# Performance work log

Measured on AMD Instinct MI355X. Metric: run time of the kernel, lower is better.

Reference implementation:

```python
import jax, jax.numpy as jnp
import numpy as np

DMODEL = 1024
NHEAD = 16
DHEAD = DMODEL // NHEAD

def _layernorm(x, g, b, eps=1e-5):
    mu = jnp.mean(x, axis=-1, keepdims=True)
    var = jnp.var(x, axis=-1, keepdims=True)
    return (x - mu) * jax.lax.rsqrt(var + eps) * g + b

def setup_inputs() -> dict:
    key = jax.random.key(0)
    ks = jax.random.split(key, 12)
    b, lq, lv, d = 2, 2048, 2048, DMODEL
    s = 1.0 / np.sqrt(d)
    return {
        "q": jax.random.normal(ks[0], (b, lq, d), jnp.float32),
        "k": jax.random.normal(ks[1], (b, lv, d), jnp.float32),
        "v": jax.random.normal(ks[2], (b, lv, d), jnp.float32),
        "qln_g": jnp.ones((d,), jnp.float32),
        "qln_b": jnp.zeros((d,), jnp.float32),
        "kvln_g": jnp.ones((d,), jnp.float32),
        "kvln_b": jnp.zeros((d,), jnp.float32),
        "Wq": jax.random.normal(ks[3], (d, d), jnp.float32) * s,
        "Wk": jax.random.normal(ks[4], (d, d), jnp.float32) * s,
        "Wv": jax.random.normal(ks[5], (d, d), jnp.float32) * s,
        "Wg": jax.random.normal(ks[6], (d, d), jnp.float32) * s,
        "bg": jnp.zeros((d,), jnp.float32),
        "Wo": jax.random.normal(ks[7], (d, d), jnp.float32) * s,
    }

def reference(q, k, v, qln_g, qln_b, kvln_g, kvln_b, Wq, Wk, Wv, Wg, bg, Wo):
    b, lq, d = q.shape
    lv = v.shape[1]
    qn = _layernorm(q, qln_g, qln_b)           # [b, lq, d]
    q_ = qn @ Wq.T
    kk = _layernorm(k, kvln_g, kvln_b) @ Wk.T
    vv = _layernorm(v, kvln_g, kvln_b) @ Wv.T
    qh = q_.reshape(b, lq, NHEAD, DHEAD)       # bqhd
    kh = kk.reshape(b, lv, NHEAD, DHEAD)
    vh = vv.reshape(b, lv, NHEAD, DHEAD)
    scores = jnp.einsum('bqhd,bkhd->bhqk', qh, kh) / np.sqrt(DHEAD)
    attn = jax.nn.softmax(scores, axis=-1)
    y = jnp.einsum('bhqk,bkhd->bqhd', attn, vh).reshape(b, lq, d)
    g = jax.nn.sigmoid(qn @ Wg.T + bg)
    return (y * g) @ Wo.T
```

## Files before the change

### kernel.cpp

```cpp
#include <hip/hip_runtime.h>
#include <hip/hip_bf16.h>

#define DMODEL 1024
#define NHEAD  16
#define DHEAD  64
#define BATCH  2
#define LQ     2048
#define LV     2048
#define ROWS   (BATCH*LQ)
#define WELEMS (DMODEL*DMODEL)
#define BH     (BATCH*NHEAD)

typedef short bf16x8 __attribute__((ext_vector_type(8)));
typedef float f32x4  __attribute__((ext_vector_type(4)));

__device__ __forceinline__ float bf2f(unsigned short s) {
    union { unsigned u; float f; } v; v.u = ((unsigned)s) << 16;
    return v.f;
}
__device__ __forceinline__ unsigned pk_bf(float a, float b) {
    union { __hip_bfloat162 h; unsigned u; } c;
    c.h = __float22bfloat162_rn(make_float2(a, b));
    return c.u;
}

__device__ __forceinline__ void cp16_g2l(const void* g, void* l) {
    __builtin_amdgcn_global_load_lds(
        (const __attribute__((address_space(1))) void*)g,
        (__attribute__((address_space(3))) void*)l,
        16, 0, 0);
}

#define QSCALE (0.125f * 1.4426950408889634f)

__global__ __launch_bounds__(256) void prep_kernel(
    const float* q, const float* k, const float* v,
    const float* qg, const float* qb, const float* kvg, const float* kvb,
    const float* Wq, const float* Wk, const float* Wv, const float* Wg, const float* Wo,
    unsigned short* qn, unsigned short* kn, unsigned short* vn, unsigned short* wb)
{
    __shared__ float rs[4], rq[4];
    int z = blockIdx.y;
    if (z < 5) {
        if (blockIdx.x >= WELEMS / 1024) return;
        const float* srcs[5] = {Wq, Wk, Wv, Wg, Wo};
        const float* s = srcs[z];
        unsigned short* d = wb + (size_t)z * WELEMS;
        int i = (blockIdx.x * 256 + threadIdx.x) * 4;
        float4 x = *(const float4*)(s + i);
        uint2 o = make_uint2(pk_bf(x.x, x.y), pk_bf(x.z, x.w));
        *(uint2*)(d + i) = o;
        return;
    }
    int row = blockIdx.x;
    const float *x, *gp, *bp; unsigned short* o;
    if      (z == 5) { x = q; gp = qg;  bp = qb;  o = qn; }
    else if (z == 6) { x = k; gp = kvg; bp = kvb; o = kn; }
    else             { x = v; gp = kvg; bp = kvb; o = vn; }

    int col = threadIdx.x * 4;
    float4 xv = *(const float4*)(x + (size_t)row * DMODEL + col);
    float s  = xv.x + xv.y + xv.z + xv.w;
    float sq = xv.x*xv.x + xv.y*xv.y + xv.z*xv.z + xv.w*xv.w;
    #pragma unroll
    for (int off = 1; off < 64; off <<= 1) { s += __shfl_xor(s, off); sq += __shfl_xor(sq, off); }

    int wave = threadIdx.x >> 6, lane = threadIdx.x & 63;
    if (lane == 0) { rs[wave] = s; rq[wave] = sq; }
    __syncthreads();
    float ts = rs[0] + rs[1] + rs[2] + rs[3];
    float tq = rq[0] + rq[1] + rq[2] + rq[3];
    float mu  = ts * (1.0f / DMODEL);
    float var = tq * (1.0f / DMODEL) - mu * mu;
    float inv = rsqrtf(var + 1e-5f);

    float4 gv = *(const float4*)(gp + col);
    float4 bv = *(const float4*)(bp + col);
    float r0 = (xv.x - mu) * inv * gv.x + bv.x;
    float r1 = (xv.y - mu) * inv * gv.y + bv.y;
    float r2 = (xv.z - mu) * inv * gv.z + bv.z;
    float r3 = (xv.w - mu) * inv * gv.w + bv.w;
    *(uint2*)(o + (size_t)row * DMODEL + col) = make_uint2(pk_bf(r0, r1), pk_bf(r2, r3));
}

template<int MODE>
__device__ __forceinline__ void gemm_bt_core(
    const unsigned short* A, const unsigned short* Bw,
    unsigned short* Obf, float* Of32, const float* bias, float scale,
    unsigned short* Al, unsigned short* Bl, int bm, int bn)
{
    int tid  = threadIdx.x;
    int wave = tid >> 6, lane = tid & 63, quad = lane >> 4, L = lane & 15;
    int wm = wave >> 1, wn = wave & 1;

    int srow = wave * 16 + (lane >> 2);
    int scol = (lane & 3) * 8;
    const unsigned short* gA = A  + (size_t)(bm * 128 + srow) * DMODEL + scol;
    const unsigned short* gB = Bw + (size_t)(bn * 128 + srow) * DMODEL + scol;
    int lofs0 = wave * 16 * 32;
    int lofs1 = (64 + wave * 16) * 32;

    f32x4 acc[4][4];
    #pragma unroll
    for (int i = 0; i < 4; ++i)
        #pragma unroll
        for (int j = 0; j < 4; ++j) acc[i][j] = (f32x4){0.f, 0.f, 0.f, 0.f};

    cp16_g2l(gA,               Al + lofs0);
    cp16_g2l(gA + 64 * DMODEL, Al + lofs1);
    cp16_g2l(gB,               Bl + lofs0);
    cp16_g2l(gB + 64 * DMODEL, Bl + lofs1);

    int buf = 0;
    for (int k0 = 0; k0 < DMODEL; k0 += 32, buf ^= 1) {
        __syncthreads();
        if (k0 + 32 < DMODEL) {
            int nb = (buf ^ 1) * (128 * 32);
            cp16_g2l(gA + k0 + 32,               Al + nb + lofs0);
            cp16_g2l(gA + 64 * DMODEL + k0 + 32, Al + nb + lofs1);
            cp16_g2l(gB + k0 + 32,               Bl + nb + lofs0);
            cp16_g2l(gB + 64 * DMODEL + k0 + 32, Bl + nb + lofs1);
        }
        const unsigned short* Ab = Al + buf * (128 * 32);
        const unsigned short* Bb = Bl + buf * (128 * 32);
        bf16x8 af[4], bfr[4];
        #pragma unroll
        for (int i = 0; i < 4; ++i)
            af[i] = *(const bf16x8*)&Ab[(wm * 64 + i * 16 + L) * 32 + quad * 8];
        #pragma unroll
        for (int j = 0; j < 4; ++j)
            bfr[j] = *(const bf16x8*)&Bb[(wn * 64 + j * 16 + L) * 32 + quad * 8];
        #pragma unroll
        for (int i = 0; i < 4; ++i)
            #pragma unroll
            for (int j = 0; j < 4; ++j) {
                if (MODE == 3)
                    acc[i][j] = __builtin_amdgcn_mfma_f32_16x16x32_bf16(af[i], bfr[j], acc[i][j], 0, 0, 0);
                else
                    acc[i][j] = __builtin_amdgcn_mfma_f32_16x16x32_bf16(bfr[j], af[i], acc[i][j], 0, 0, 0);
            }
    }

    #pragma unroll
    for (int i = 0; i < 4; ++i) {
        #pragma unroll
        for (int j = 0; j < 4; ++j) {
            f32x4 a = acc[i][j];
            if (MODE == 3) {
                int gcol  = bn * 128 + wn * 64 + j * 16 + L;
                int grow0 = bm * 128 + wm * 64 + i * 16 + quad * 4;
                int b = grow0 >> 11, key0 = grow0 & 2047;
                int h = gcol >> 6,   dd   = gcol & 63;
                uint2 o = make_uint2(pk_bf(a[0], a[1]), pk_bf(a[2], a[3]));
                *(uint2*)&Obf[(((size_t)(b * NHEAD + h) * DHEAD + dd) << 11) + key0] = o;
            } else {
                int grow  = bm * 128 + wm * 64 + i * 16 + L;
                int gcol0 = bn * 128 + wn * 64 + j * 16 + quad * 4;
                size_t idx = (size_t)grow * DMODEL + gcol0;
                if (MODE == 0) {
                    uint2 o = make_uint2(pk_bf(a[0] * scale, a[1] * scale),
                                         pk_bf(a[2] * scale, a[3] * scale));
                    *(uint2*)&Obf[idx] = o;
                } else if (MODE == 1) {
                    float4 bv = *(const float4*)&bias[gcol0];
                    float s0 = 1.0f / (1.0f + __expf(-(a[0] + bv.x)));
                    float s1 = 1.0f / (1.0f + __expf(-(a[1] + bv.y)));
                    float s2 = 1.0f / (1.0f + __expf(-(a[2] + bv.z)));
                    float s3 = 1.0f / (1.0f + __expf(-(a[3] + bv.w)));
                    *(uint2*)&Obf[idx] = make_uint2(pk_bf(s0, s1), pk_bf(s2, s3));
                } else {
                    *(f32x4*)&Of32[idx] = a;
                }
            }
        }
    }
}

__device__ __forceinline__ void xcd_map(int& bm, int& bn) {
    int f = blockIdx.y * 8 + blockIdx.x;
    int xcd = f & 7, s = f >> 3;
    bn = s & 7;
    bm = ((s >> 3) << 3) | xcd;
}

__global__ __launch_bounds__(256) void gemm_batched_kernel(
    const unsigned short* qn, const unsigned short* kn, const unsigned short* vn,
    const unsigned short* wb,
    unsigned short* qs, unsigned short* kkp, unsigned short* vt, unsigned short* gate,
    const float* bg)
{
    __shared__ __align__(16) unsigned short Al[2 * 128 * 32];
    __shared__ __align__(16) unsigned short Bl[2 * 128 * 32];
    int bm, bn; xcd_map(bm, bn);
    switch (blockIdx.z) {
        case 0:  gemm_bt_core<0>(qn, wb + 0 * WELEMS, qs,   nullptr, nullptr, QSCALE, Al, Bl, bm, bn); break;
        case 1:  gemm_bt_core<0>(kn, wb + 1 * WELEMS, kkp,  nullptr, nullptr, 1.0f,   Al, Bl, bm, bn); break;
        case 2:  gemm_bt_core<3>(vn, wb + 2 * WELEMS, vt,   nullptr, nullptr, 1.0f,   Al, Bl, bm, bn); break;
        default: gemm_bt_core<1>(qn, wb + 3 * WELEMS, gate, nullptr, bg,      1.0f,   Al, Bl, bm, bn); break;
    }
}

__global__ __launch_bounds__(256) void gemm_f32out_kernel(
    const unsigned short* A, const unsigned short* Bw, float* O)
{
    __shared__ __align__(16) unsigned short Al[2 * 128 * 32];
    __shared__ __align__(16) unsigned short Bl[2 * 128 * 32];
    int bm, bn; xcd_map(bm, bn);
    gemm_bt_core<2>(A, Bw, nullptr, O, nullptr, 1.0f, Al, Bl, bm, bn);
}

__global__ __launch_bounds__(256, 4) void attn_kernel(
    const unsigned short* qs, const unsigned short* kk, const unsigned short* vt,
    const unsigned short* gate, unsigned short* yg)
{
    __shared__ __align__(16) unsigned short Kl[2 * 64 * 64];
    __shared__ __align__(16) unsigned short Vl[2 * 64 * 64];

    int tid  = threadIdx.x;
    int wave = tid >> 6, lane = tid & 63, quad = lane >> 4, L = lane & 15;

    int f  = blockIdx.y * 32 + blockIdx.x;
    int bh = (f & 7) * 4 + ((f >> 3) & 3);
    int qt = f >> 5;
    int bb = bh >> 4, h = bh & 15;
    int q0 = qt * 64;

    const unsigned short* Qb =
        qs + ((size_t)(bb * LQ + q0 + wave * 16 + L)) * DMODEL + h * DHEAD;
    bf16x8 aq0 = *(const bf16x8*)(Qb + quad * 8);
    bf16x8 aq1 = *(const bf16x8*)(Qb + 32 + quad * 8);

    f32x4 acc[4];
    #pragma unroll
    for (int nt = 0; nt < 4; ++nt) acc[nt] = (f32x4){0.f, 0.f, 0.f, 0.f};
    f32x4 lacc = (f32x4){0.f, 0.f, 0.f, 0.f};
    bf16x8 ones;
    #pragma unroll
    for (int j = 0; j < 8; ++j) ones[j] = (short)0x3F80;

    int rloc = lane >> 3;
    int c16  = (lane & 7) ^ rloc;
    int key0 = (wave & 1) * 32 + (rloc >> 2) * 8 + (wave >> 1) * 4 + (rloc & 3);

    const unsigned short* gK = kk + (size_t)bb * LV * DMODEL + h * DHEAD
                                  + (size_t)key0 * DMODEL + c16 * 8;
    const unsigned short* gV = vt + ((size_t)((bb * NHEAD + h) * DHEAD
                                  + wave * 16 + rloc)) * LV + c16 * 8;
    char* KlB = (char*)Kl;
    char* VlB = (char*)Vl;
    int dst0 = wave * 2048;

    cp16_g2l(gK,               KlB + dst0);
    cp16_g2l(gK + 16 * DMODEL, KlB + dst0 + 1024);
    cp16_g2l(gV,               VlB + dst0);
    cp16_g2l(gV + 8 * LV,      VlB + dst0 + 1024);

    int sl0 = (quad ^ (L & 7)) * 8;
    int buf = 0;
    for (int it = 0; it < LV / 64; ++it, buf ^= 1) {
        __syncthreads();
        if (it + 1 < LV / 64) {
            gK += 64 * DMODEL; gV += 64;
            int nb = (buf ^ 1) * 8192 + dst0;
            cp16_g2l(gK,               KlB + nb);
            cp16_g2l(gK + 16 * DMODEL, KlB + nb + 1024);
            cp16_g2l(gV,               VlB + nb);
            cp16_g2l(gV + 8 * LV,      VlB + nb + 1024);
        }
        const unsigned short* Kb = Kl + buf * 4096;
        const unsigned short* Vb = Vl + buf * 4096;

        f32x4 zz[4];
        __builtin_amdgcn_s_setprio(1);
        #pragma unroll
        for (int kt = 0; kt < 4; ++kt) {
            bf16x8 bk0 = *(const bf16x8*)&Kb[(kt * 16 + L) * 64 + sl0];
            bf16x8 bk1 = *(const bf16x8*)&Kb[(kt * 16 + L) * 64 + (sl0 ^ 32)];
            f32x4 z = (f32x4){0.f, 0.f, 0.f, 0.f};
            z = __builtin_amdgcn_mfma_f32_16x16x32_bf16(bk0, aq0, z, 0, 0, 0);
            z = __builtin_amdgcn_mfma_f32_16x16x32_bf16(bk1, aq1, z, 0, 0, 0);
            zz[kt] = z;
        }
        __builtin_amdgcn_s_setprio(0);

        union { unsigned u[4]; bf16x8 h; } pa0, pa1;
        pa0.u[0] = pk_bf(__builtin_amdgcn_exp2f(zz[0][0]), __builtin_amdgcn_exp2f(zz[0][1]));
        pa0.u[1] = pk_bf(__builtin_amdgcn_exp2f(zz[0][2]), __builtin_amdgcn_exp2f(zz[0][3]));
        pa0.u[2] = pk_bf(__builtin_amdgcn_exp2f(zz[2][0]), __builtin_amdgcn_exp2f(zz[2][1]));
        pa0.u[3] = pk_bf(__builtin_amdgcn_exp2f(zz[2][2]), __builtin_amdgcn_exp2f(zz[2][3]));
        pa1.u[0] = pk_bf(__builtin_amdgcn_exp2f(zz[1][0]), __builtin_amdgcn_exp2f(zz[1][1]));
        pa1.u[1] = pk_bf(__builtin_amdgcn_exp2f(zz[1][2]), __builtin_amdgcn_exp2f(zz[1][3]));
        pa1.u[2] = pk_bf(__builtin_amdgcn_exp2f(zz[3][0]), __builtin_amdgcn_exp2f(zz[3][1]));
        pa1.u[3] = pk_bf(__builtin_amdgcn_exp2f(zz[3][2]), __builtin_amdgcn_exp2f(zz[3][3]));

        __builtin_amdgcn_s_setprio(1);
        lacc = __builtin_amdgcn_mfma_f32_16x16x32_bf16(ones, pa0.h, lacc, 0, 0, 0);
        lacc = __builtin_amdgcn_mfma_f32_16x16x32_bf16(ones, pa1.h, lacc, 0, 0, 0);
        #pragma unroll
        for (int nt = 0; nt < 4; ++nt) {
            bf16x8 vb0 = *(const bf16x8*)&Vb[(nt * 16 + L) * 64 + sl0];
            bf16x8 vb1 = *(const bf16x8*)&Vb[(nt * 16 + L) * 64 + (sl0 ^ 32)];
            acc[nt] = __builtin_amdgcn_mfma_f32_16x16x32_bf16(vb0, pa0.h, acc[nt], 0, 0, 0);
            acc[nt] = __builtin_amdgcn_mfma_f32_16x16x32_bf16(vb1, pa1.h, acc[nt], 0, 0, 0);
        }
        __builtin_amdgcn_s_setprio(0);
    }

    float inv_l = 1.0f / lacc[0];
    size_t rb = ((size_t)(bb * LQ + q0 + wave * 16 + L)) * DMODEL + h * DHEAD;
    #pragma unroll
    for (int nt = 0; nt < 4; ++nt) {
        size_t idx = rb + nt * 16 + quad * 4;
        ushort4 g = *(const ushort4*)&gate[idx];
        float y0 = acc[nt][0] * inv_l * bf2f(g.x);
        float y1 = acc[nt][1] * inv_l * bf2f(g.y);
        float y2 = acc[nt][2] * inv_l * bf2f(g.z);
        float y3 = acc[nt][3] * inv_l * bf2f(g.w);
        *(uint2*)&yg[idx] = make_uint2(pk_bf(y0, y1), pk_bf(y2, y3));
    }
}

extern "C" void kernel_launch(void* const* d_in, const int* in_sizes, int n_in,
                              void* d_out, int out_size, void* d_ws, size_t ws_size,
                              hipStream_t stream)
{
    const float* q      = (const float*)d_in[0];
    const float* k      = (const float*)d_in[1];
    const float* v      = (const float*)d_in[2];
    const float* qln_g  = (const float*)d_in[3];
    const float* qln_b  = (const float*)d_in[4];
    const float* kvln_g = (const float*)d_in[5];
    const float* kvln_b = (const float*)d_in[6];
    const float* Wq     = (const float*)d_in[7];
    const float* Wk     = (const float*)d_in[8];
    const float* Wv     = (const float*)d_in[9];
    const float* Wg     = (const float*)d_in[10];
    const float* bg     = (const float*)d_in[11];
    const float* Wo     = (const float*)d_in[12];
    float* out = (float*)d_out;

    const size_t T8 = (size_t)ROWS * DMODEL * 2;
    char* ws = (char*)d_ws;
    unsigned short* qn   = (unsigned short*)(ws + 0 * T8);
    unsigned short* kn   = (unsigned short*)(ws + 1 * T8);
    unsigned short* vn   = (unsigned short*)(ws + 2 * T8);
    unsigned short* qs   = (unsigned short*)(ws + 3 * T8);
    unsigned short* kkp  = (unsigned short*)(ws + 4 * T8);
    unsigned short* vt   = (unsigned short*)(ws + 5 * T8);
    unsigned short* gate = (unsigned short*)(ws + 6 * T8);
    unsigned short* yg   = (unsigned short*)(ws + 7 * T8);
    unsigned short* wb   = (unsigned short*)(ws + 8 * T8);

    prep_kernel<<<dim3(ROWS, 8), 256, 0, stream>>>(
        q, k, v, qln_g, qln_b, kvln_g, kvln_b, Wq, Wk, Wv, Wg, Wo, qn, kn, vn, wb);
    gemm_batched_kernel<<<dim3(DMODEL / 128, ROWS / 128, 4), 256, 0, stream>>>(
        qn, kn, vn, wb, qs, kkp, vt, gate, bg);
    attn_kernel<<<dim3(32, 32), 256, 0, stream>>>(qs, kkp, vt, gate, yg);
    gemm_f32out_kernel<<<dim3(DMODEL / 128, ROWS / 128), 256, 0, stream>>>(yg, wb + 4 * WELEMS, out);
}
```

Before: 249.2 us.

## Replace batched QKV/gate GEMM with 256x256-tile 512-thread pipelined kernel

```diff
diff --git a/kernel.cpp b/kernel.cpp
--- a/kernel.cpp
+++ b/kernel.cpp
@@ -84,6 +84,150 @@
 }
 
 template<int MODE>
+__device__ __forceinline__ void gemm256_core(
+    const unsigned short* A, const unsigned short* Bw,
+    unsigned short* Obf, const float* bias, float scale,
+    unsigned short* Al, unsigned short* Bl, int bm, int bn)
+{
+    int tid  = threadIdx.x;
+    int w = tid >> 6, l = tid & 63, quad = l >> 4, L = l & 15;
+    int wm = w >> 2, wn = w & 3;
+
+    int srow = w * 16 + (l >> 2);
+    int scol = (l & 3) * 8;
+    const unsigned short* gA = A  + (size_t)(bm * 256 + srow) * DMODEL + scol;
+    const unsigned short* gB = Bw + (size_t)(bn * 256 + srow) * DMODEL + scol;
+    int dst = w * 512;
+
+    f32x4 acc[8][4];
+    #pragma unroll
+    for (int i = 0; i < 8; ++i)
+        #pragma unroll
+        for (int j = 0; j < 4; ++j) acc[i][j] = (f32x4){0.f, 0.f, 0.f, 0.f};
+
+    cp16_g2l(gB,                     Bl + dst);
+    cp16_g2l(gB + 128 * DMODEL,      Bl + 4096 + dst);
+    cp16_g2l(gA,                     Al + dst);
+    cp16_g2l(gA + 128 * DMODEL,      Al + 4096 + dst);
+    cp16_g2l(gB + 32,                Bl + 8192 + dst);
+    cp16_g2l(gB + 32 + 128 * DMODEL, Bl + 8192 + 4096 + dst);
+    asm volatile("s_waitcnt vmcnt(2)" ::: "memory");
+    __builtin_amdgcn_s_barrier();
+
+    const int NT = DMODEL / 32;
+    for (int t = 0; t < NT; ++t) {
+        int d = t & 1;
+        const unsigned short* Ab = Al + d * 8192 + wm * 4096;
+        const unsigned short* Bb = Bl + d * 8192 + (wn >> 1) * 4096;
+        int brow = (wn & 1) * 64;
+
+        bf16x8 bfr[4], af[4];
+        #pragma unroll
+        for (int j = 0; j < 4; ++j)
+            bfr[j] = *(const bf16x8*)&Bb[(brow + j * 16 + L) * 32 + quad * 8];
+        #pragma unroll
+        for (int i2 = 0; i2 < 4; ++i2)
+            af[i2] = *(const bf16x8*)&Ab[(i2 * 16 + L) * 32 + quad * 8];
+        if (t + 1 < NT) {
+            int nd = (t + 1) & 1;
+            const unsigned short* sA = gA + (t + 1) * 32;
+            cp16_g2l(sA,                Al + nd * 8192 + dst);
+            cp16_g2l(sA + 128 * DMODEL, Al + nd * 8192 + 4096 + dst);
+        }
+        __builtin_amdgcn_s_barrier();
+        __builtin_amdgcn_s_setprio(1);
+        #pragma unroll
+        for (int i2 = 0; i2 < 4; ++i2)
+            #pragma unroll
+            for (int j = 0; j < 4; ++j) {
+                if (MODE == 3)
+                    acc[i2][j] = __builtin_amdgcn_mfma_f32_16x16x32_bf16(af[i2], bfr[j], acc[i2][j], 0, 0, 0);
+                else
+                    acc[i2][j] = __builtin_amdgcn_mfma_f32_16x16x32_bf16(bfr[j], af[i2], acc[i2][j], 0, 0, 0);
+            }
+        __builtin_amdgcn_s_setprio(0);
+        __builtin_amdgcn_s_barrier();
+
+        #pragma unroll
+        for (int i2 = 0; i2 < 4; ++i2)
+            af[i2] = *(const bf16x8*)&Ab[((64 + i2 * 16) + L) * 32 + quad * 8];
+        if (t + 2 < NT) {
+            int nd = t & 1;
+            const unsigned short* sB = gB + (t + 2) * 32;
+            cp16_g2l(sB,                Bl + nd * 8192 + dst);
+            cp16_g2l(sB + 128 * DMODEL, Bl + nd * 8192 + 4096 + dst);
+        }
+        __builtin_amdgcn_s_barrier();
+        __builtin_amdgcn_s_setprio(1);
+        #pragma unroll
+        for (int i2 = 0; i2 < 4; ++i2)
+            #pragma unroll
+            for (int j = 0; j < 4; ++j) {
+                if (MODE == 3)
+                    acc[4 + i2][j] = __builtin_amdgcn_mfma_f32_16x16x32_bf16(af[i2], bfr[j], acc[4 + i2][j], 0, 0, 0);
+                else
+                    acc[4 + i2][j] = __builtin_amdgcn_mfma_f32_16x16x32_bf16(bfr[j], af[i2], acc[4 + i2][j], 0, 0, 0);
+            }
+        __builtin_amdgcn_s_setprio(0);
+        if (t + 2 < NT) asm volatile("s_waitcnt vmcnt(2)" ::: "memory");
+        else            asm volatile("s_waitcnt vmcnt(0)" ::: "memory");
+        __builtin_amdgcn_s_barrier();
+    }
+
+    #pragma unroll
+    for (int i = 0; i < 8; ++i) {
+        #pragma unroll
+        for (int j = 0; j < 4; ++j) {
+            f32x4 a = acc[i][j];
+            if (MODE == 3) {
+                int gcol  = bn * 256 + wn * 64 + j * 16 + L;
+                int grow0 = bm * 256 + wm * 128 + i * 16 + quad * 4;
+                int b = grow0 >> 11, key0 = grow0 & 2047;
+                int h = gcol >> 6,   dd   = gcol & 63;
+                uint2 o = make_uint2(pk_bf(a[0], a[1]), pk_bf(a[2], a[3]));
+                *(uint2*)&Obf[(((size_t)(b * NHEAD + h) * DHEAD + dd) << 11) + key0] = o;
+            } else {
+                int grow  = bm * 256 + wm * 128 + i * 16 + L;
+                int gcol0 = bn * 256 + wn * 64 + j * 16 + quad * 4;
+                size_t idx = (size_t)grow * DMODEL + gcol0;
+                if (MODE == 0) {
+                    uint2 o = make_uint2(pk_bf(a[0] * scale, a[1] * scale),
+                                         pk_bf(a[2] * scale, a[3] * scale));
+                    *(uint2*)&Obf[idx] = o;
+                } else {
+                    float4 bv = *(const float4*)&bias[gcol0];
+                    float s0 = 1.0f / (1.0f + __expf(-(a[0] + bv.x)));
+                    float s1 = 1.0f / (1.0f + __expf(-(a[1] + bv.y)));
+                    float s2 = 1.0f / (1.0f + __expf(-(a[2] + bv.z)));
+                    float s3 = 1.0f / (1.0f + __expf(-(a[3] + bv.w)));
+                    *(uint2*)&Obf[idx] = make_uint2(pk_bf(s0, s1), pk_bf(s2, s3));
+                }
+            }
+        }
+    }
+}
+
+__global__ __launch_bounds__(512, 2) void gemm256_kernel(
+    const unsigned short* qn, const unsigned short* kn, const unsigned short* vn,
+    const unsigned short* wb,
+    unsigned short* qs, unsigned short* kkp, unsigned short* vt, unsigned short* gate,
+    const float* bg)
+{
+    __shared__ __align__(16) unsigned short Al[2 * 2 * 128 * 32];
+    __shared__ __align__(16) unsigned short Bl[2 * 2 * 128 * 32];
+    int f = blockIdx.x, xcd = f & 7, s = f >> 3;
+    int z  = xcd & 3;
+    int bm = ((xcd >> 2) << 3) | (s >> 2);
+    int bn = s & 3;
+    switch (z) {
+        case 0:  gemm256_core<0>(qn, wb + 0 * WELEMS, qs,   nullptr, QSCALE, Al, Bl, bm, bn); break;
+        case 1:  gemm256_core<0>(kn, wb + 1 * WELEMS, kkp,  nullptr, 1.0f,   Al, Bl, bm, bn); break;
+        case 2:  gemm256_core<3>(vn, wb + 2 * WELEMS, vt,   nullptr, 1.0f,   Al, Bl, bm, bn); break;
+        default: gemm256_core<1>(qn, wb + 3 * WELEMS, gate, bg,      1.0f,   Al, Bl, bm, bn); break;
+    }
+}
+
+template<int MODE>
 __device__ __forceinline__ void gemm_bt_core(
     const unsigned short* A, const unsigned short* Bw,
     unsigned short* Obf, float* Of32, const float* bias, float scale,
@@ -146,31 +290,15 @@
         #pragma unroll
         for (int j = 0; j < 4; ++j) {
             f32x4 a = acc[i][j];
-            if (MODE == 3) {
-                int gcol  = bn * 128 + wn * 64 + j * 16 + L;
-                int grow0 = bm * 128 + wm * 64 + i * 16 + quad * 4;
-                int b = grow0 >> 11, key0 = grow0 & 2047;
-                int h = gcol >> 6,   dd   = gcol & 63;
-                uint2 o = make_uint2(pk_bf(a[0], a[1]), pk_bf(a[2], a[3]));
-                *(uint2*)&Obf[(((size_t)(b * NHEAD + h) * DHEAD + dd) << 11) + key0] = o;
-            } else {
-                int grow  = bm * 128 + wm * 64 + i * 16 + L;
-                int gcol0 = bn * 128 + wn * 64 + j * 16 + quad * 4;
-                size_t idx = (size_t)grow * DMODEL + gcol0;
-                if (MODE == 0) {
-                    uint2 o = make_uint2(pk_bf(a[0] * scale, a[1] * scale),
-                                         pk_bf(a[2] * scale, a[3] * scale));
-                    *(uint2*)&Obf[idx] = o;
-                } else if (MODE == 1) {
-                    float4 bv = *(const float4*)&bias[gcol0];
-                    float s0 = 1.0f / (1.0f + __expf(-(a[0] + bv.x)));
-                    float s1 = 1.0f / (1.0f + __expf(-(a[1] + bv.y)));
-                    float s2 = 1.0f / (1.0f + __expf(-(a[2] + bv.z)));
-                    float s3 = 1.0f / (1.0f + __expf(-(a[3] + bv.w)));
-                    *(uint2*)&Obf[idx] = make_uint2(pk_bf(s0, s1), pk_bf(s2, s3));
-                } else {
-                    *(f32x4*)&Of32[idx] = a;
-                }
+            int grow  = bm * 128 + wm * 64 + i * 16 + L;
+            int gcol0 = bn * 128 + wn * 64 + j * 16 + quad * 4;
+            size_t idx = (size_t)grow * DMODEL + gcol0;
+            if (MODE == 2) {
+                *(f32x4*)&Of32[idx] = a;
+            } else if (MODE == 0) {
+                uint2 o = make_uint2(pk_bf(a[0] * scale, a[1] * scale),
+                                     pk_bf(a[2] * scale, a[3] * scale));
+                *(uint2*)&Obf[idx] = o;
             }
         }
     }
@@ -181,23 +309,6 @@
     int xcd = f & 7, s = f >> 3;
     bn = s & 7;
     bm = ((s >> 3) << 3) | xcd;
-}
-
-__global__ __launch_bounds__(256) void gemm_batched_kernel(
-    const unsigned short* qn, const unsigned short* kn, const unsigned short* vn,
-    const unsigned short* wb,
-    unsigned short* qs, unsigned short* kkp, unsigned short* vt, unsigned short* gate,
-    const float* bg)
-{
-    __shared__ __align__(16) unsigned short Al[2 * 128 * 32];
-    __shared__ __align__(16) unsigned short Bl[2 * 128 * 32];
-    int bm, bn; xcd_map(bm, bn);
-    switch (blockIdx.z) {
-        case 0:  gemm_bt_core<0>(qn, wb + 0 * WELEMS, qs,   nullptr, nullptr, QSCALE, Al, Bl, bm, bn); break;
-        case 1:  gemm_bt_core<0>(kn, wb + 1 * WELEMS, kkp,  nullptr, nullptr, 1.0f,   Al, Bl, bm, bn); break;
-        case 2:  gemm_bt_core<3>(vn, wb + 2 * WELEMS, vt,   nullptr, nullptr, 1.0f,   Al, Bl, bm, bn); break;
-        default: gemm_bt_core<1>(qn, wb + 3 * WELEMS, gate, nullptr, bg,      1.0f,   Al, Bl, bm, bn); break;
-    }
 }
 
 __global__ __launch_bounds__(256) void gemm_f32out_kernel(
@@ -353,7 +464,7 @@
 
     prep_kernel<<<dim3(ROWS, 8), 256, 0, stream>>>(
         q, k, v, qln_g, qln_b, kvln_g, kvln_b, Wq, Wk, Wv, Wg, Wo, qn, kn, vn, wb);
-    gemm_batched_kernel<<<dim3(DMODEL / 128, ROWS / 128, 4), 256, 0, stream>>>(
+    gemm256_kernel<<<dim3(256), 512, 0, stream>>>(
         qn, kn, vn, wb, qs, kkp, vt, gate, bg);
     attn_kernel<<<dim3(32, 32), 256, 0, stream>>>(qs, kkp, vt, gate, yg);
     gemm_f32out_kernel<<<dim3(DMODEL / 128, ROWS / 128), 256, 0, stream>>>(yg, wb + 4 * WELEMS, out);
```

Result: no change. 245.0 us (-1.7%).
